# Kernel tuning notes

Measured on AMD Instinct MI355X. Metric: run time of the kernel, lower is better.

## Reference

```python
import jax, jax.numpy as jnp
import numpy as np
from jax import lax

B, S, D, N_ORIG, GROUP_DIM, R = 8, 4096, 512, 4096, 64, 1024
EPS_MERGE = 1e-8
EPS_NORM = 1e-12  # F.normalize eps


def setup_inputs() -> dict:
    key = jax.random.key(0)
    k1, k2, k3 = jax.random.split(key, 3)
    x = jax.random.normal(k1, (B, S, D), dtype=jnp.float32)
    source = jax.random.normal(k2, (B, S, N_ORIG), dtype=jnp.float32)
    position_ids = jnp.arange(B * S, dtype=jnp.int32).reshape(B, S)
    # nn.Linear(dim, group_dim, bias=False) weight: (group_dim, dim)
    W = jax.random.normal(k3, (GROUP_DIM, D), dtype=jnp.float32) / np.sqrt(D)
    return {"x": x, "source": source, "position_ids": position_ids, "W": W, "r": R}


def _greedy_select(sim, r):
    """Greedy disjoint adjacent-pair selection; returns bool (S-1,) edge mask."""
    Sm1 = sim.shape[0]
    order = jnp.argsort(-sim, stable=True)  # matches torch.argsort(-sim, stable=True)

    def step(carry, p):
        used, sel, cnt = carry
        ok = (~used[p]) & (~used[p + 1]) & (cnt < r)
        used = used.at[p].set(used[p] | ok)
        used = used.at[p + 1].set(used[p + 1] | ok)
        sel = sel.at[p].set(ok)
        return (used, sel, cnt + ok.astype(jnp.int32)), None

    init = (jnp.zeros(Sm1 + 1, dtype=bool), jnp.zeros(Sm1, dtype=bool), jnp.int32(0))
    (_, sel, _), _ = lax.scan(step, init, order)
    return sel


def _merge_one(x, src, pos, sim, norms, r):
    Sl = x.shape[0]
    sel = _greedy_select(sim, r)  # sel[p] True => merge pair (p, p+1)
    w = norms[:, None]
    # weighted merge of adjacent pairs, written at position i = p
    merged = (w[:-1] * x[:-1] + w[1:] * x[1:]) / (w[:-1] + w[1:] + EPS_MERGE)
    x_out = jnp.concatenate([jnp.where(sel[:, None], merged, x[:-1]), x[-1:]], axis=0)
    src_out = src.at[:-1].add(jnp.where(sel[:, None], src[1:], 0.0))
    drop = jnp.concatenate([jnp.zeros(1, dtype=bool), sel])  # token p+1 dropped
    idx = jnp.arange(Sl)
    keep_order = jnp.argsort(jnp.where(drop, Sl + idx, idx))[: Sl - r]  # kept, in order
    return x_out[keep_order], src_out[keep_order], pos[keep_order]


def reference(x, source, position_ids, W, r):
    g = jnp.einsum("bsd,gd->bsg", x, W)  # group projection
    gnorms = jnp.linalg.norm(g, axis=-1)  # (B, S)
    g_unit = g / jnp.maximum(gnorms[..., None], EPS_NORM)
    sim = jnp.sum(g_unit[:, :-1] * g_unit[:, 1:], axis=-1)  # (B, S-1)
    merge = lambda xb, sb, pb, simb, nb: _merge_one(xb, sb, pb, simb, nb, r)
    return jax.vmap(merge)(x, source, position_ids, sim, gnorms)
```

## Files before the change

### kernel.cpp

```cpp
#include <hip/hip_runtime.h>
#include <hip/hip_bf16.h>
#include <stdint.h>

#define B_ 8
#define S_ 4096
#define D_ 512
#define G_ 64
#define R_ 1024
#define NO_ 4096
#define SO_ 3072
#define EPS_MERGE 1e-8f
#define EPS_NORM 1e-12f

#define WS_G     0ull
#define WS_GN    8388608ull
#define WS_KEYS  8519680ull
#define WS_KEPT  8781824ull

__global__ __launch_bounds__(256) void k1_proj(const float* __restrict__ x,
                                               const float* __restrict__ W,
                                               float* __restrict__ g,
                                               float* __restrict__ gn) {
  __shared__ float xs[32][132];
  __shared__ float wc[32][68];
  const int tid = threadIdx.x;
  const int gt  = tid & 15;
  const int rt  = tid >> 4;
  const int rb  = blockIdx.x * 128;
  const int g0  = gt * 4;
  const int r0  = rt * 8;
  float acc[8][4];
#pragma unroll
  for (int r = 0; r < 8; ++r)
#pragma unroll
    for (int j = 0; j < 4; ++j) acc[r][j] = 0.f;

  for (int kc = 0; kc < 16; ++kc) {
    const int kbase = kc * 32;
    __syncthreads();
#pragma unroll
    for (int i = 0; i < 4; ++i) {
      int f4i = tid + i * 256;
      int row_l = f4i >> 3;
      int kq = f4i & 7;
      const float4 v = *reinterpret_cast<const float4*>(
          &x[(size_t)(rb + row_l) * D_ + kbase + kq * 4]);
      xs[kq * 4 + 0][row_l] = v.x;
      xs[kq * 4 + 1][row_l] = v.y;
      xs[kq * 4 + 2][row_l] = v.z;
      xs[kq * 4 + 3][row_l] = v.w;
    }
#pragma unroll
    for (int i = 0; i < 2; ++i) {
      int f4i = tid + i * 256;
      int gg = f4i >> 3;
      int kq = f4i & 7;
      const float4 v = *reinterpret_cast<const float4*>(
          &W[(size_t)gg * D_ + kbase + kq * 4]);
      wc[kq * 4 + 0][gg] = v.x;
      wc[kq * 4 + 1][gg] = v.y;
      wc[kq * 4 + 2][gg] = v.z;
      wc[kq * 4 + 3][gg] = v.w;
    }
    __syncthreads();
#pragma unroll
    for (int k = 0; k < 32; ++k) {
      const float4 wv = *reinterpret_cast<const float4*>(&wc[k][g0]);
      const float4 xa = *reinterpret_cast<const float4*>(&xs[k][r0]);
      const float4 xb = *reinterpret_cast<const float4*>(&xs[k][r0 + 4]);
      const float xr[8] = {xa.x, xa.y, xa.z, xa.w, xb.x, xb.y, xb.z, xb.w};
#pragma unroll
      for (int r = 0; r < 8; ++r) {
        acc[r][0] = fmaf(xr[r], wv.x, acc[r][0]);
        acc[r][1] = fmaf(xr[r], wv.y, acc[r][1]);
        acc[r][2] = fmaf(xr[r], wv.z, acc[r][2]);
        acc[r][3] = fmaf(xr[r], wv.w, acc[r][3]);
      }
    }
  }
#pragma unroll
  for (int r = 0; r < 8; ++r) {
    const int row = rb + r0 + r;
    float4 v;
    v.x = acc[r][0]; v.y = acc[r][1]; v.z = acc[r][2]; v.w = acc[r][3];
    *reinterpret_cast<float4*>(&g[(size_t)row * G_ + g0]) = v;
    float ss = v.x * v.x + v.y * v.y + v.z * v.z + v.w * v.w;
    ss += __shfl_xor(ss, 1);
    ss += __shfl_xor(ss, 2);
    ss += __shfl_xor(ss, 4);
    ss += __shfl_xor(ss, 8);
    if (gt == 0) gn[row] = sqrtf(ss);
  }
}

__global__ __launch_bounds__(256) void k2_sim(const float* __restrict__ g,
                                              const float* __restrict__ gn,
                                              unsigned long long* __restrict__ prio) {
  const int wid = blockIdx.x * 4 + (threadIdx.x >> 6);
  const int lane = threadIdx.x & 63;
  if (wid >= B_ * (S_ - 1)) return;
  const int b = wid / (S_ - 1);
  const int e = wid - b * (S_ - 1);
  const size_t row = (size_t)b * S_ + e;
  const float a = g[row * G_ + lane];
  const float c = g[(row + 1) * G_ + lane];
  float p = a * c;
  p += __shfl_xor(p, 1);
  p += __shfl_xor(p, 2);
  p += __shfl_xor(p, 4);
  p += __shfl_xor(p, 8);
  p += __shfl_xor(p, 16);
  p += __shfl_xor(p, 32);
  if (lane == 0) {
    const float n0 = fmaxf(gn[row], EPS_NORM);
    const float n1 = fmaxf(gn[row + 1], EPS_NORM);
    const float sim = p / (n0 * n1);
    const unsigned int u = __float_as_uint(sim);
    const unsigned int m = (u & 0x80000000u) ? ~u : (u | 0x80000000u);
    prio[(size_t)b * S_ + e] =
        ((unsigned long long)m << 32) | (unsigned long long)(unsigned int)(4095 - e);
  }
}

__global__ __launch_bounds__(256) void k3_match(const unsigned long long* __restrict__ prio,
                                                unsigned int* __restrict__ kept) {
  __shared__ unsigned long long pr[4096];
  __shared__ unsigned int stw[258];
  __shared__ int hist[256];
  __shared__ int wsum[4];
  __shared__ int sh_flag;
  __shared__ int sh_need;
  __shared__ unsigned long long sh_prefix;

  const int tid = threadIdx.x;
  const int b = blockIdx.x;

#pragma unroll
  for (int j = 0; j < 16; ++j) {
    const int e = tid + j * 256;
    pr[e] = (e < 4095) ? prio[(size_t)b * S_ + e] : 0ull;
  }
  if (tid == 0) {
    stw[0] = 0xAAAAAAAAu;
    stw[257] = 0xAAAAAAAAu;
    sh_flag = 0; sh_need = R_; sh_prefix = 0ull;
  }
  stw[1 + tid] = (tid == 255) ? 0x80000000u : 0u;
  __syncthreads();

  unsigned int cl = 0, cr = 0;
#pragma unroll
  for (int j = 0; j < 16; ++j) {
    const int e = tid * 16 + j;
    const unsigned long long pe = pr[e];
    const bool L = (e == 0) || (pe > pr[e - 1]);
    const bool R = (e >= 4094) || (pe > pr[e + 1]);
    cl |= (L ? 1u : 0u) << (2 * j);
    cr |= (R ? 1u : 0u) << (2 * j);
  }

  for (;;) {
    __syncthreads();
    if (tid == 0) sh_flag = 0;
    __syncthreads();
    unsigned int u = stw[1 + tid];
    const unsigned int lw = stw[tid];
    const unsigned int rw = stw[2 + tid];
    const unsigned int linb = (lw >> 30) & 1u;
    const unsigned int loutb = (lw >> 31) & 1u;
    const unsigned int rinb = (rw & 1u) << 30;
    const unsigned int routb = ((rw >> 1) & 1u) << 30;
    bool changed = false;
    for (;;) {
      const unsigned int a = u & 0x55555555u;
      const unsigned int d = (u >> 1) & 0x55555555u;
      const unsigned int lin = (a << 2) | linb;
      const unsigned int lout = (d << 2) | loutb;
      const unsigned int rin = (a >> 2) | rinb;
      const unsigned int rout = (d >> 2) | routb;
      const unsigned int undec = ~(a | d) & 0x55555555u;
      const unsigned int nout = undec & (lin | rin);
      const unsigned int nin = undec & ~lin & ~rin & (lout | cl) & (rout | cr);
      if (!(nin | nout)) break;
      u |= nin | (nout << 1);
      changed = true;
    }
    if (changed) { stw[1 + tid] = u; sh_flag = 1; }
    __syncthreads();
    if (sh_flag == 0) break;
  }

  const unsigned int inw = stw[1 + tid] & 0x55555555u;

#pragma unroll 1
  for (int level = 0; level < 8; ++level) {
    const int shift = 56 - 8 * level;
    __syncthreads();
    hist[tid] = 0;
    __syncthreads();
    const unsigned long long pref = sh_prefix;
#pragma unroll
    for (int j = 0; j < 16; ++j) {
      if (!((inw >> (2 * j)) & 1u)) continue;
      const int e = tid * 16 + j;
      const unsigned long long p = pr[e];
      const bool match = (level == 0) || ((p >> (shift + 8)) == (pref >> (shift + 8)));
      if (match) atomicAdd(&hist[(int)((p >> shift) & 255ull)], 1);
    }
    __syncthreads();
    if (tid < 64) {
      const int lane = tid;
      const int need = sh_need;
      const int h0 = hist[lane * 4 + 0], h1 = hist[lane * 4 + 1];
      const int h2 = hist[lane * 4 + 2], h3 = hist[lane * 4 + 3];
      const int gsum = h0 + h1 + h2 + h3;
      int s = gsum;
#pragma unroll
      for (int off = 1; off < 64; off <<= 1) {
        const int v = __shfl_down(s, off);
        if (lane + off < 64) s += v;
      }
      const int suffAbove = s - gsum;
      if (suffAbove < need && s >= need) {
        const int hh[4] = {h0, h1, h2, h3};
        int cum = suffAbove;
        for (int q = 3; q >= 0; --q) {
          cum += hh[q];
          if (cum >= need) {
            sh_prefix = pref | ((unsigned long long)(lane * 4 + q) << shift);
            sh_need = need - (cum - hh[q]);
            break;
          }
        }
      }
    }
    __syncthreads();
  }
  const unsigned long long thresh = sh_prefix;
  const unsigned int previnw = stw[tid] & 0x55555555u;

  int c = 0;
  unsigned int kpbits = 0;
#pragma unroll
  for (int j = 0; j < 16; ++j) {
    const int s = tid * 16 + j;
    bool selprev = false;
    if (s > 0) {
      const unsigned int ib =
          (j == 0) ? ((previnw >> 30) & 1u) : ((inw >> (2 * (j - 1))) & 1u);
      selprev = ib && (pr[s - 1] >= thresh);
    }
    if (!selprev) { kpbits |= 1u << j; ++c; }
  }
  const int lane = tid & 63, w = tid >> 6;
  int v = c;
#pragma unroll
  for (int off = 1; off < 64; off <<= 1) {
    const int t2 = __shfl_up(v, off);
    if (lane >= off) v += t2;
  }
  if (lane == 63) wsum[w] = v;
  __syncthreads();
  if (tid == 0) {
    int run = 0;
    for (int q = 0; q < 4; ++q) { const int t3 = wsum[q]; wsum[q] = run; run += t3; }
  }
  __syncthreads();
  int pos = (v - c) + wsum[w];
#pragma unroll
  for (int j = 0; j < 16; ++j) {
    if ((kpbits >> j) & 1u) {
      const int s = tid * 16 + j;
      const unsigned int m =
          (((inw >> (2 * j)) & 1u) && pr[s] >= thresh) ? 0x80000000u : 0u;
      kept[b * SO_ + pos] = (unsigned int)s | m;
      ++pos;
    }
  }
}

__global__ __launch_bounds__(128) void k4_x(const float* __restrict__ x,
                                            const float* __restrict__ gn,
                                            const int* __restrict__ posid,
                                            const unsigned int* __restrict__ kept,
                                            float* __restrict__ outx,
                                            float* __restrict__ outpos) {
  const int blk = blockIdx.x;
  const int b = blk / SO_;
  const int j = blk - b * SO_;
  const unsigned int ent = kept[b * SO_ + j];
  const int s = (int)(ent & 0x7FFFFFFFu);
  const bool m = (ent & 0x80000000u) != 0u;
  const size_t rin = (size_t)b * S_ + s;
  const size_t rout = (size_t)b * SO_ + j;
  const int t = threadIdx.x;
  if (t == 0) outpos[rout] = (float)posid[rin];
  float4 a = *reinterpret_cast<const float4*>(&x[rin * D_ + t * 4]);
  float4 o;
  if (m) {
    const float w0 = gn[rin], w1 = gn[rin + 1];
    const float4 c2 = *reinterpret_cast<const float4*>(&x[(rin + 1) * D_ + t * 4]);
    const float den = w0 + w1 + EPS_MERGE;
    o.x = (w0 * a.x + w1 * c2.x) / den;
    o.y = (w0 * a.y + w1 * c2.y) / den;
    o.z = (w0 * a.z + w1 * c2.z) / den;
    o.w = (w0 * a.w + w1 * c2.w) / den;
  } else {
    o = a;
  }
  *reinterpret_cast<float4*>(&outx[rout * D_ + t * 4]) = o;
}

__global__ __launch_bounds__(256) void k5_src(const float* __restrict__ src,
                                              const unsigned int* __restrict__ kept,
                                              float* __restrict__ outs) {
  const int blk = blockIdx.x;
  const int b = blk / SO_;
  const int j = blk - b * SO_;
  const unsigned int ent = kept[b * SO_ + j];
  const int s = (int)(ent & 0x7FFFFFFFu);
  const bool m = (ent & 0x80000000u) != 0u;
  const size_t rin = ((size_t)b * S_ + s) * NO_;
  const size_t rout = ((size_t)b * SO_ + j) * NO_;
  const int t = threadIdx.x;
#pragma unroll
  for (int it = 0; it < 4; ++it) {
    const int f4 = t + it * 256;
    float4 a = *reinterpret_cast<const float4*>(&src[rin + (size_t)f4 * 4]);
    if (m) {
      const float4 c2 =
          *reinterpret_cast<const float4*>(&src[rin + NO_ + (size_t)f4 * 4]);
      a.x += c2.x; a.y += c2.y; a.z += c2.z; a.w += c2.w;
    }
    *reinterpret_cast<float4*>(&outs[rout + (size_t)f4 * 4]) = a;
  }
}

extern "C" void kernel_launch(void* const* d_in, const int* in_sizes, int n_in,
                              void* d_out, int out_size, void* d_ws, size_t ws_size,
                              hipStream_t stream) {
  (void)in_sizes; (void)n_in; (void)out_size; (void)ws_size;
  const float* x = (const float*)d_in[0];
  const float* src = (const float*)d_in[1];
  const int* posid = (const int*)d_in[2];
  const float* W = (const float*)d_in[3];

  char* ws = (char*)d_ws;
  float* g = (float*)(ws + WS_G);
  float* gn = (float*)(ws + WS_GN);
  unsigned long long* prio = (unsigned long long*)(ws + WS_KEYS);
  unsigned int* kept = (unsigned int*)(ws + WS_KEPT);

  float* outx = (float*)d_out;
  float* outs = outx + (size_t)B_ * SO_ * D_;
  float* outpos = outs + (size_t)B_ * SO_ * NO_;

  hipLaunchKernelGGL(k1_proj, dim3(256), dim3(256), 0, stream, x, W, g, gn);
  hipLaunchKernelGGL(k2_sim, dim3((B_ * (S_ - 1) + 3) / 4), dim3(256), 0, stream, g, gn, prio);
  hipLaunchKernelGGL(k3_match, dim3(B_), dim3(256), 0, stream, prio, kept);
  hipLaunchKernelGGL(k4_x, dim3(B_ * SO_), dim3(128), 0, stream, x, gn, posid, kept,
                     outx, outpos);
  hipLaunchKernelGGL(k5_src, dim3(B_ * SO_), dim3(256), 0, stream, src, kept, outs);
}
```

Before: 277.3 us.

## Fuse gather kernels, prefetch projection tiles, early-exit radix select, nontemporal src copy

```diff
diff --git a/kernel.cpp b/kernel.cpp
--- a/kernel.cpp
+++ b/kernel.cpp
@@ -11,6 +11,8 @@
 #define SO_ 3072
 #define EPS_MERGE 1e-8f
 #define EPS_NORM 1e-12f
+
+typedef float f4v __attribute__((ext_vector_type(4)));
 
 #define WS_G     0ull
 #define WS_GN    8388608ull
@@ -29,6 +31,24 @@
   const int rb  = blockIdx.x * 128;
   const int g0  = gt * 4;
   const int r0  = rt * 8;
+  const int kq4 = (tid & 7) * 4;
+  const int rl0 = tid >> 3;
+
+  const float* xp[4];
+  const float* wp[2];
+#pragma unroll
+  for (int i = 0; i < 4; ++i)
+    xp[i] = &x[(size_t)(rb + rl0 + i * 32) * D_ + kq4];
+#pragma unroll
+  for (int i = 0; i < 2; ++i)
+    wp[i] = &W[(size_t)(rl0 + i * 32) * D_ + kq4];
+
+  float4 px[4], pw[2];
+#pragma unroll
+  for (int i = 0; i < 4; ++i) px[i] = *reinterpret_cast<const float4*>(xp[i]);
+#pragma unroll
+  for (int i = 0; i < 2; ++i) pw[i] = *reinterpret_cast<const float4*>(wp[i]);
+
   float acc[8][4];
 #pragma unroll
   for (int r = 0; r < 8; ++r)
@@ -36,31 +56,31 @@
     for (int j = 0; j < 4; ++j) acc[r][j] = 0.f;
 
   for (int kc = 0; kc < 16; ++kc) {
-    const int kbase = kc * 32;
     __syncthreads();
 #pragma unroll
     for (int i = 0; i < 4; ++i) {
-      int f4i = tid + i * 256;
-      int row_l = f4i >> 3;
-      int kq = f4i & 7;
-      const float4 v = *reinterpret_cast<const float4*>(
-          &x[(size_t)(rb + row_l) * D_ + kbase + kq * 4]);
-      xs[kq * 4 + 0][row_l] = v.x;
-      xs[kq * 4 + 1][row_l] = v.y;
-      xs[kq * 4 + 2][row_l] = v.z;
-      xs[kq * 4 + 3][row_l] = v.w;
+      const int rl = rl0 + i * 32;
+      xs[kq4 + 0][rl] = px[i].x;
+      xs[kq4 + 1][rl] = px[i].y;
+      xs[kq4 + 2][rl] = px[i].z;
+      xs[kq4 + 3][rl] = px[i].w;
     }
 #pragma unroll
     for (int i = 0; i < 2; ++i) {
-      int f4i = tid + i * 256;
-      int gg = f4i >> 3;
-      int kq = f4i & 7;
-      const float4 v = *reinterpret_cast<const float4*>(
-          &W[(size_t)gg * D_ + kbase + kq * 4]);
-      wc[kq * 4 + 0][gg] = v.x;
-      wc[kq * 4 + 1][gg] = v.y;
-      wc[kq * 4 + 2][gg] = v.z;
-      wc[kq * 4 + 3][gg] = v.w;
+      const int gg = rl0 + i * 32;
+      wc[kq4 + 0][gg] = pw[i].x;
+      wc[kq4 + 1][gg] = pw[i].y;
+      wc[kq4 + 2][gg] = pw[i].z;
+      wc[kq4 + 3][gg] = pw[i].w;
+    }
+    if (kc < 15) {
+      const int off = (kc + 1) * 32;
+#pragma unroll
+      for (int i = 0; i < 4; ++i)
+        px[i] = *reinterpret_cast<const float4*>(xp[i] + off);
+#pragma unroll
+      for (int i = 0; i < 2; ++i)
+        pw[i] = *reinterpret_cast<const float4*>(wp[i] + off);
     }
     __syncthreads();
 #pragma unroll
@@ -130,7 +150,10 @@
   __shared__ int wsum[4];
   __shared__ int sh_flag;
   __shared__ int sh_need;
+  __shared__ int sh_exact;
   __shared__ unsigned long long sh_prefix;
+  __shared__ unsigned long long sh_tmin;
+  __shared__ unsigned long long sh_tmax;
 
   const int tid = threadIdx.x;
   const int b = blockIdx.x;
@@ -144,6 +167,7 @@
     stw[0] = 0xAAAAAAAAu;
     stw[257] = 0xAAAAAAAAu;
     sh_flag = 0; sh_need = R_; sh_prefix = 0ull;
+    sh_exact = 0; sh_tmin = ~0ull; sh_tmax = 0ull;
   }
   stw[1 + tid] = (tid == 255) ? 0x80000000u : 0u;
   __syncthreads();
@@ -192,6 +216,7 @@
 
   const unsigned int inw = stw[1 + tid] & 0x55555555u;
 
+  int exitmode = 0;
 #pragma unroll 1
   for (int level = 0; level < 8; ++level) {
     const int shift = 56 - 8 * level;
@@ -202,8 +227,7 @@
 #pragma unroll
     for (int j = 0; j < 16; ++j) {
       if (!((inw >> (2 * j)) & 1u)) continue;
-      const int e = tid * 16 + j;
-      const unsigned long long p = pr[e];
+      const unsigned long long p = pr[tid * 16 + j];
       const bool match = (level == 0) || ((p >> (shift + 8)) == (pref >> (shift + 8)));
       if (match) atomicAdd(&hist[(int)((p >> shift) & 255ull)], 1);
     }
@@ -227,16 +251,44 @@
         for (int q = 3; q >= 0; --q) {
           cum += hh[q];
           if (cum >= need) {
+            const int need2 = need - (cum - hh[q]);
             sh_prefix = pref | ((unsigned long long)(lane * 4 + q) << shift);
-            sh_need = need - (cum - hh[q]);
+            sh_need = need2;
+            if (need2 == hh[q]) sh_exact = 1;
+            else if (need2 == 1) sh_exact = 2;
             break;
           }
         }
       }
     }
     __syncthreads();
-  }
-  const unsigned long long thresh = sh_prefix;
+    const int ex = sh_exact;
+    if (ex) {
+      exitmode = ex;
+      const unsigned long long pref2 = sh_prefix;
+      unsigned long long best = (ex == 1) ? ~0ull : 0ull;
+#pragma unroll
+      for (int j = 0; j < 16; ++j) {
+        if (!((inw >> (2 * j)) & 1u)) continue;
+        const unsigned long long p = pr[tid * 16 + j];
+        if ((p >> shift) == (pref2 >> shift))
+          best = (ex == 1) ? (best < p ? best : p) : (best > p ? best : p);
+      }
+#pragma unroll
+      for (int off = 1; off < 64; off <<= 1) {
+        const unsigned long long o = __shfl_xor(best, off);
+        best = (ex == 1) ? (best < o ? best : o) : (best > o ? best : o);
+      }
+      if ((tid & 63) == 0) {
+        if (ex == 1) atomicMin(&sh_tmin, best);
+        else atomicMax(&sh_tmax, best);
+      }
+      __syncthreads();
+      break;
+    }
+  }
+  const unsigned long long thresh =
+      (exitmode == 1) ? sh_tmin : (exitmode == 2) ? sh_tmax : sh_prefix;
   const unsigned int previnw = stw[tid] & 0x55555555u;
 
   int c = 0;
@@ -279,61 +331,56 @@
   }
 }
 
-__global__ __launch_bounds__(128) void k4_x(const float* __restrict__ x,
-                                            const float* __restrict__ gn,
-                                            const int* __restrict__ posid,
-                                            const unsigned int* __restrict__ kept,
-                                            float* __restrict__ outx,
-                                            float* __restrict__ outpos) {
+__global__ __launch_bounds__(256) void k45_gather(const float* __restrict__ src,
+                                                  const float* __restrict__ x,
+                                                  const float* __restrict__ gn,
+                                                  const int* __restrict__ posid,
+                                                  const unsigned int* __restrict__ kept,
+                                                  float* __restrict__ outs,
+                                                  float* __restrict__ outx,
+                                                  float* __restrict__ outpos) {
   const int blk = blockIdx.x;
   const int b = blk / SO_;
   const int j = blk - b * SO_;
   const unsigned int ent = kept[b * SO_ + j];
   const int s = (int)(ent & 0x7FFFFFFFu);
   const bool m = (ent & 0x80000000u) != 0u;
-  const size_t rin = (size_t)b * S_ + s;
-  const size_t rout = (size_t)b * SO_ + j;
+  const size_t rrow = (size_t)b * S_ + s;
+  const size_t orow = (size_t)b * SO_ + j;
+  const size_t rin = rrow * NO_;
+  const size_t rout = orow * NO_;
   const int t = threadIdx.x;
-  if (t == 0) outpos[rout] = (float)posid[rin];
-  float4 a = *reinterpret_cast<const float4*>(&x[rin * D_ + t * 4]);
-  float4 o;
-  if (m) {
-    const float w0 = gn[rin], w1 = gn[rin + 1];
-    const float4 c2 = *reinterpret_cast<const float4*>(&x[(rin + 1) * D_ + t * 4]);
-    const float den = w0 + w1 + EPS_MERGE;
-    o.x = (w0 * a.x + w1 * c2.x) / den;
-    o.y = (w0 * a.y + w1 * c2.y) / den;
-    o.z = (w0 * a.z + w1 * c2.z) / den;
-    o.w = (w0 * a.w + w1 * c2.w) / den;
-  } else {
-    o = a;
-  }
-  *reinterpret_cast<float4*>(&outx[rout * D_ + t * 4]) = o;
-}
-
-__global__ __launch_bounds__(256) void k5_src(const float* __restrict__ src,
-                                              const unsigned int* __restrict__ kept,
-                                              float* __restrict__ outs) {
-  const int blk = blockIdx.x;
-  const int b = blk / SO_;
-  const int j = blk - b * SO_;
-  const unsigned int ent = kept[b * SO_ + j];
-  const int s = (int)(ent & 0x7FFFFFFFu);
-  const bool m = (ent & 0x80000000u) != 0u;
-  const size_t rin = ((size_t)b * S_ + s) * NO_;
-  const size_t rout = ((size_t)b * SO_ + j) * NO_;
-  const int t = threadIdx.x;
+
 #pragma unroll
   for (int it = 0; it < 4; ++it) {
     const int f4 = t + it * 256;
-    float4 a = *reinterpret_cast<const float4*>(&src[rin + (size_t)f4 * 4]);
+    f4v a = __builtin_nontemporal_load(
+        reinterpret_cast<const f4v*>(&src[rin + (size_t)f4 * 4]));
     if (m) {
-      const float4 c2 =
-          *reinterpret_cast<const float4*>(&src[rin + NO_ + (size_t)f4 * 4]);
-      a.x += c2.x; a.y += c2.y; a.z += c2.z; a.w += c2.w;
-    }
-    *reinterpret_cast<float4*>(&outs[rout + (size_t)f4 * 4]) = a;
-  }
+      const f4v c2 = __builtin_nontemporal_load(
+          reinterpret_cast<const f4v*>(&src[rin + NO_ + (size_t)f4 * 4]));
+      a += c2;
+    }
+    __builtin_nontemporal_store(a, reinterpret_cast<f4v*>(&outs[rout + (size_t)f4 * 4]));
+  }
+
+  if (t < 128) {
+    float4 a = *reinterpret_cast<const float4*>(&x[rrow * D_ + t * 4]);
+    float4 o;
+    if (m) {
+      const float w0 = gn[rrow], w1 = gn[rrow + 1];
+      const float4 c2 = *reinterpret_cast<const float4*>(&x[(rrow + 1) * D_ + t * 4]);
+      const float den = w0 + w1 + EPS_MERGE;
+      o.x = (w0 * a.x + w1 * c2.x) / den;
+      o.y = (w0 * a.y + w1 * c2.y) / den;
+      o.z = (w0 * a.z + w1 * c2.z) / den;
+      o.w = (w0 * a.w + w1 * c2.w) / den;
+    } else {
+      o = a;
+    }
+    *reinterpret_cast<float4*>(&outx[orow * D_ + t * 4]) = o;
+  }
+  if (t == 0) outpos[orow] = (float)posid[rrow];
 }
 
 extern "C" void kernel_launch(void* const* d_in, const int* in_sizes, int n_in,
@@ -358,7 +405,6 @@
   hipLaunchKernelGGL(k1_proj, dim3(256), dim3(256), 0, stream, x, W, g, gn);
   hipLaunchKernelGGL(k2_sim, dim3((B_ * (S_ - 1) + 3) / 4), dim3(256), 0, stream, g, gn, prio);
   hipLaunchKernelGGL(k3_match, dim3(B_), dim3(256), 0, stream, prio, kept);
-  hipLaunchKernelGGL(k4_x, dim3(B_ * SO_), dim3(128), 0, stream, x, gn, posid, kept,
-                     outx, outpos);
-  hipLaunchKernelGGL(k5_src, dim3(B_ * SO_), dim3(256), 0, stream, src, kept, outs);
+  hipLaunchKernelGGL(k45_gather, dim3(B_ * SO_), dim3(256), 0, stream, src, x, gn,
+                     posid, kept, outs, outx, outpos);
 }
```

New measurement: 228.8 us. 1.21x faster.
